# Kernel optimization log

Hardware: AMD Instinct MI355X
Metric: run time of the kernel (lower is better)

The kernel has to match this reference:

```python
import jax, jax.numpy as jnp
import numpy as np
import math

B, Q, C, H, L, P = 8, 900, 256, 8, 4, 4
D = C // H  # head_dim = 32
SPATIAL = np.array([[100, 100], [50, 50], [25, 25], [13, 13]], dtype=np.int64)
AREAS = SPATIAL[:, 0] * SPATIAL[:, 1]
STARTS = np.concatenate([[0], np.cumsum(AREAS)[:-1]]).astype(np.int64)
S = int(AREAS.sum())  # 13294


def _xavier(k, i, o, scale=1.0):
    return jax.random.normal(k, (i, o), jnp.float32) * scale * (2.0 / (i + o)) ** 0.5


def setup_inputs() -> dict:
    key = jax.random.key(0)
    ks = jax.random.split(key, 16)
    inp = {}
    inp['query'] = jax.random.normal(ks[0], (B, Q, C), jnp.float32)
    inp['reference_points'] = jax.random.uniform(ks[1], (B, Q, L, 2), jnp.float32)
    inp['input_flatten'] = jax.random.normal(ks[2], (B, S, C), jnp.float32)
    inp['object_shape'] = jax.random.uniform(ks[3], (B, Q, 2), jnp.float32) * 0.3 + 0.02
    inp['input_spatial_shapes'] = jnp.asarray(SPATIAL)
    inp['input_level_start_index'] = jnp.asarray(STARTS)
    # learned parameters (torch zero-inits offset/attn weights; use small random for a nontrivial baseline)
    inp['w_q'] = _xavier(ks[4], C, C); inp['b_q'] = jnp.zeros((C,), jnp.float32)
    inp['w_v'] = _xavier(ks[5], C, C); inp['b_v'] = jnp.zeros((C,), jnp.float32)
    inp['w_o'] = _xavier(ks[6], C, C); inp['b_o'] = jnp.zeros((C,), jnp.float32)
    inp['w_off1'] = _xavier(ks[7], C + 2, C); inp['b_off1'] = jnp.zeros((C,), jnp.float32)
    inp['w_off2'] = _xavier(ks[8], C, H * L * P * 2, scale=0.05)
    inp['b_off2'] = jax.random.normal(ks[9], (H * L * P * 2,), jnp.float32) * 0.02
    inp['w_ax'] = _xavier(ks[10], C, H * L * P, scale=0.1); inp['b_ax'] = jnp.zeros((H * L * P,), jnp.float32)
    inp['w_ay'] = _xavier(ks[11], C, H * L * P, scale=0.1); inp['b_ay'] = jnp.zeros((H * L * P,), jnp.float32)
    # spectral basis per original init: head h uses freq pi*(h+1)/H over arange(D)
    freq = (np.arange(1, H + 1, dtype=np.float32)[:, None] * math.pi / H) * np.arange(D, dtype=np.float32)[None, :]
    inp['basis_x'] = jnp.asarray(np.cos(freq), jnp.float32)
    inp['basis_y'] = jnp.asarray(np.sin(freq), jnp.float32)
    return inp


def _bilinear_sample(v, locs):
    """v: (B,S,H,D); locs: (B,Q,H,L,P,2) in [0,1]. grid_sample semantics: align_corners=False, zeros padding.
    Returns (B,Q,H,L,P,D)."""
    levels = []
    for lvl in range(L):
        Hl, Wl = int(SPATIAL[lvl, 0]), int(SPATIAL[lvl, 1])
        start = int(STARTS[lvl])
        v_l = v[:, start:start + Hl * Wl]  # (B, Hl*Wl, H, D)
        loc = locs[:, :, :, lvl]  # (B,Q,H,P,2)
        # align_corners=False: pixel coord = loc * size - 0.5
        x = loc[..., 0] * Wl - 0.5
        y = loc[..., 1] * Hl - 0.5
        x0 = jnp.floor(x); y0 = jnp.floor(y)
        fx = x - x0; fy = y - y0
        x0i = x0.astype(jnp.int32); y0i = y0.astype(jnp.int32)
        acc = jnp.zeros((B, Q, H, P, D), jnp.float32)
        corners = [(0, 0, (1 - fx) * (1 - fy)), (1, 0, fx * (1 - fy)),
                   (0, 1, (1 - fx) * fy), (1, 1, fx * fy)]
        for dx, dy, w in corners:
            xi = x0i + dx; yi = y0i + dy
            valid = (xi >= 0) & (xi < Wl) & (yi >= 0) & (yi < Hl)
            idx = jnp.clip(yi, 0, Hl - 1) * Wl + jnp.clip(xi, 0, Wl - 1)  # (B,Q,H,P)
            idx_t = idx.transpose(0, 1, 3, 2).reshape(B, Q * P, H)[..., None]  # (B,Q*P,H,1)
            g = jnp.take_along_axis(v_l, idx_t, axis=1)  # (B,Q*P,H,D)
            g = g.reshape(B, Q, P, H, D).transpose(0, 1, 3, 2, 4)  # (B,Q,H,P,D)
            acc = acc + g * (w * valid.astype(jnp.float32))[..., None]
        levels.append(acc)
    return jnp.stack(levels, axis=3)  # (B,Q,H,L,P,D)


def reference(query, reference_points, input_flatten, input_spatial_shapes, input_level_start_index,
              object_shape, w_q, b_q, w_v, b_v, w_o, b_o, w_off1, b_off1, w_off2, b_off2,
              w_ax, b_ax, w_ay, b_ay, basis_x, basis_y):
    q = query @ w_q + b_q  # (B,Q,C)
    v = (input_flatten @ w_v + b_v).reshape(B, S, H, D)
    q_shape = jnp.concatenate([q, object_shape], axis=-1)  # (B,Q,C+2)
    hid = jax.nn.relu(q_shape @ w_off1 + b_off1)
    offsets = (hid @ w_off2 + b_off2).reshape(B, Q, H, L, P, 2)
    offsets = offsets * object_shape[:, :, None, None, None, :]
    ref = reference_points[:, :, None, :, None, :]  # (B,Q,1,L,1,2)
    locs = jnp.clip(ref + offsets, 0.0, 1.0)  # (B,Q,H,L,P,2)
    q_heads = q.reshape(B, Q, H, D)
    spec = jnp.einsum('bqhd,hd->bqh', q_heads, basis_x) * jnp.einsum('bqhd,hd->bqh', q_heads, basis_y)
    attn_x = (q @ w_ax + b_ax).reshape(B, Q, H, L, P)
    attn_y = (q @ w_ay + b_ay).reshape(B, Q, H, L, P)
    attn = attn_x * attn_y + spec[..., None, None]
    attn = jax.nn.softmax(attn.reshape(B, Q, H, L * P), axis=-1).reshape(B, Q, H, L, P)
    sampled = _bilinear_sample(v, locs)  # (B,Q,H,L,P,D)
    out = (sampled * attn[..., None]).sum(axis=(3, 4)).reshape(B, Q, C)
    return out @ w_o + b_o  # dropout is identity in eval
```

## Files before the change

kernel.cpp:

```cpp
#include <hip/hip_runtime.h>
#include <hip/hip_bf16.h>
#include <math.h>

constexpr int B_ = 8, Q_ = 900;
constexpr int S_ = 13294;
constexpr int BQ = 7200;
constexpr int BS = 106352;

typedef __bf16 bf16x8 __attribute__((ext_vector_type(8)));
typedef float  f32x4  __attribute__((ext_vector_type(4)));

#define WAITLGKM0 asm volatile("s_waitcnt lgkmcnt(0)" ::: "memory")
#define SCHEDB    __builtin_amdgcn_sched_barrier(0)
#define BAR       __builtin_amdgcn_s_barrier()
#define CFENCE    asm volatile("" ::: "memory")

__device__ __forceinline__ void load_lds16(const void* g, void* lds) {
    __builtin_amdgcn_global_load_lds(
        (const __attribute__((address_space(1))) void*)g,
        (__attribute__((address_space(3))) void*)lds, 16, 0, 0);
}

__global__ __launch_bounds__(256)
void transpose_all(const float* __restrict__ wv, const float* __restrict__ wo,
                   const float* __restrict__ woff1, const float* __restrict__ woff2,
                   const float* __restrict__ wax, const float* __restrict__ way,
                   __bf16* __restrict__ tv, __bf16* __restrict__ to_,
                   __bf16* __restrict__ toff2, __bf16* __restrict__ tcat)
{
    const int bi = blockIdx.x;
    __shared__ float tile[32][33];
    const int tx = threadIdx.x & 31, ty = threadIdx.x >> 5;

    const float* src; __bf16* dst; int k0, n0, scol, sN = 256;
    if (bi < 192) {
        const int wid = bi >> 6, t = bi & 63;
        k0 = (t & 7) * 32; n0 = (t >> 3) * 32; scol = n0;
        if      (wid == 0) { src = wv;    dst = tv;    }
        else if (wid == 1) { src = wo;    dst = to_;   }
        else               { src = woff2; dst = toff2; }
    } else {
        const int t = bi - 192;
        k0 = (t & 7) * 32; n0 = (t >> 3) * 32;
        dst = tcat;
        if      (n0 < 128) { src = wax;   scol = n0;       sN = 128; }
        else if (n0 < 256) { src = way;   scol = n0 - 128; sN = 128; }
        else               { src = woff1; scol = n0 - 256; sN = 256; }
    }

    #pragma unroll
    for (int i = 0; i < 4; ++i)
        tile[ty + 8 * i][tx] = src[(size_t)(k0 + ty + 8 * i) * sN + scol + tx];
    __syncthreads();
    #pragma unroll
    for (int i = 0; i < 4; ++i)
        dst[(size_t)(n0 + ty + 8 * i) * 256 + k0 + tx] = (__bf16)tile[tx][ty + 8 * i];
}

__global__ __launch_bounds__(256)
void combine_w(const __bf16* __restrict__ tcat, const float* __restrict__ wq,
               __bf16* __restrict__ wcomb)
{
    const int wid  = (blockIdx.x << 2) + (threadIdx.x >> 6);
    const int lane = threadIdx.x & 63;
    const int n0 = (wid >> 2) * 64, k0 = (wid & 3) * 64;
    const int l15 = lane & 15, l4 = lane >> 4;

    f32x4 acc[4][4] = {};
    #pragma unroll
    for (int s = 0; s < 8; ++s) {
        const int c0 = s * 32 + l4 * 8;
        bf16x8 am[4], bm[4];
        #pragma unroll
        for (int mi = 0; mi < 4; ++mi)
            am[mi] = *(const bf16x8*)(tcat + (size_t)(n0 + mi * 16 + l15) * 256 + c0);
        #pragma unroll
        for (int ni = 0; ni < 4; ++ni) {
            const float* wr_ = wq + (size_t)(k0 + ni * 16 + l15) * 256 + c0;
            const float4 f0 = ((const float4*)wr_)[0];
            const float4 f1 = ((const float4*)wr_)[1];
            bm[ni][0] = (__bf16)f0.x; bm[ni][1] = (__bf16)f0.y;
            bm[ni][2] = (__bf16)f0.z; bm[ni][3] = (__bf16)f0.w;
            bm[ni][4] = (__bf16)f1.x; bm[ni][5] = (__bf16)f1.y;
            bm[ni][6] = (__bf16)f1.z; bm[ni][7] = (__bf16)f1.w;
        }
        #pragma unroll
        for (int mi = 0; mi < 4; ++mi)
            #pragma unroll
            for (int ni = 0; ni < 4; ++ni)
                acc[mi][ni] = __builtin_amdgcn_mfma_f32_16x16x32_bf16(
                    am[mi], bm[ni], acc[mi][ni], 0, 0, 0);
    }
    #pragma unroll
    for (int mi = 0; mi < 4; ++mi)
        #pragma unroll
        for (int rr = 0; rr < 4; ++rr) {
            const int n = n0 + mi * 16 + l4 * 4 + rr;
            #pragma unroll
            for (int ni = 0; ni < 4; ++ni)
                wcomb[(size_t)n * 256 + k0 + ni * 16 + l15] = (__bf16)acc[mi][ni][rr];
        }
}

__global__ __launch_bounds__(256)
void combine_bias(const __bf16* __restrict__ tcat, const float* __restrict__ bq,
                  const float* __restrict__ bax, const float* __restrict__ bay,
                  const float* __restrict__ boff1, float* __restrict__ bcomb)
{
    const int n = blockIdx.x * 256 + threadIdx.x;
    float acc = (n < 128) ? bax[n] : (n < 256 ? bay[n - 128] : boff1[n - 256]);
    const __bf16* row = tcat + (size_t)n * 256;
    #pragma unroll 4
    for (int c8 = 0; c8 < 32; ++c8) {
        const bf16x8 rv = *(const bf16x8*)(row + c8 * 8);
        #pragma unroll
        for (int j = 0; j < 8; ++j) acc += bq[c8 * 8 + j] * (float)rv[j];
    }
    bcomb[n] = acc;
}

__global__ __launch_bounds__(512)
void gemm_v8(const float* __restrict__ A, const __bf16* __restrict__ Wt,
             const float* __restrict__ bias, __bf16* __restrict__ outp, int M)
{
    __shared__ float4 AsbV[2][512];
    __shared__ float4 BsbV[3][1024];
    char* const Asb_b = (char*)AsbV;
    char* const Bsb_b = (char*)BsbV;

    const int tid  = threadIdx.x;
    const int wave = tid >> 6, lane = tid & 63;
    const int wr = wave >> 2, wc = wave & 3;
    const int row0 = blockIdx.x * 128;
    const int l15 = lane & 15, l4 = lane >> 4;

    const int st_row = tid >> 2, st_kq = tid & 3;
    const int gr_cl  = min(row0 + st_row, M - 1);
    const float* Abase = A + (size_t)gr_cl * 256 + st_kq * 8;
    const int a_wo = st_row * 64 + ((st_kq ^ ((st_row >> 1) & 3)) * 16);

    int a_off[4], b_off[4];
    #pragma unroll
    for (int mi = 0; mi < 4; ++mi) {
        const int r = wr * 64 + mi * 16 + l15;
        a_off[mi] = r * 64 + (l4 ^ ((r >> 1) & 3)) * 16;
    }
    #pragma unroll
    for (int ni = 0; ni < 4; ++ni) {
        const int c = wc * 64 + ni * 16 + l15;
        b_off[ni] = c * 64 + (l4 ^ ((c >> 1) & 3)) * 16;
    }

    const __bf16* bsrc[2];
    #pragma unroll
    for (int i = 0; i < 2; ++i) {
        const int c   = (wave * 2 + i) * 64 + lane;
        const int col = c >> 2, kcp = c & 3;
        const int kc  = kcp ^ ((col >> 1) & 3);
        bsrc[i] = Wt + (size_t)col * 256 + kc * 8;
    }

    auto issueB = [&](int kt, int bbuf) {
        #pragma unroll
        for (int i = 0; i < 2; ++i)
            load_lds16(bsrc[i] + kt * 32, Bsb_b + bbuf * 16384 + (wave * 2 + i) * 1024);
    };
    auto loadA = [&](int kt, float4* g) {
        const float* ga = Abase + kt * 32;
        g[0] = ((const float4*)ga)[0];
        g[1] = ((const float4*)ga)[1];
    };
    auto writeA = [&](int abuf, const float4* g) {
        bf16x8 c0;
        c0[0] = (__bf16)g[0].x; c0[1] = (__bf16)g[0].y; c0[2] = (__bf16)g[0].z; c0[3] = (__bf16)g[0].w;
        c0[4] = (__bf16)g[1].x; c0[5] = (__bf16)g[1].y; c0[6] = (__bf16)g[1].z; c0[7] = (__bf16)g[1].w;
        *(bf16x8*)(Asb_b + abuf * 8192 + a_wo) = c0;
    };

    f32x4 acc[4][4] = {};
    float4 g[2][2];

    issueB(0, 0);
    loadA(0, g[0]);
    issueB(1, 1);
    loadA(1, g[1]);
    writeA(0, g[0]);
    WAITLGKM0; BAR; CFENCE; SCHEDB;

    #pragma unroll
    for (int u = 0; u < 8; ++u) {
        if (u + 2 <= 7) {
            loadA(u + 2, g[u & 1]);
            issueB(u + 2, (u + 2) % 3);
        }

        const char* Ab = Asb_b + (u & 1) * 8192;
        const char* Bb = Bsb_b + (u % 3) * 16384;
        bf16x8 a[4], b[4];
        #pragma unroll
        for (int mi = 0; mi < 4; ++mi) a[mi] = *(const bf16x8*)(Ab + a_off[mi]);
        #pragma unroll
        for (int ni = 0; ni < 4; ++ni) b[ni] = *(const bf16x8*)(Bb + b_off[ni]);

        #pragma unroll
        for (int mi = 0; mi < 4; ++mi)
            #pragma unroll
            for (int ni = 0; ni < 4; ++ni)
                acc[mi][ni] = __builtin_amdgcn_mfma_f32_16x16x32_bf16(
                    a[mi], b[ni], acc[mi][ni], 0, 0, 0);

        if (u + 1 <= 7) {
            writeA((u + 1) & 1, g[(u + 1) & 1]);
            WAITLGKM0; BAR; CFENCE; SCHEDB;
        }
    }

    float bb[4];
    #pragma unroll
    for (int ni = 0; ni < 4; ++ni) bb[ni] = bias[wc * 64 + ni * 16 + l15];
    #pragma unroll
    for (int mi = 0; mi < 4; ++mi) {
        #pragma unroll
        for (int rr = 0; rr < 4; ++rr) {
            const int row = row0 + wr * 64 + mi * 16 + l4 * 4 + rr;
            if (row >= M) continue;
            #pragma unroll
            for (int ni = 0; ni < 4; ++ni)
                outp[(size_t)row * 256 + wc * 64 + ni * 16 + l15] =
                    (__bf16)(acc[mi][ni][rr] + bb[ni]);
        }
    }
}

template<bool RELUHI, bool OUTBF16>
__global__ __launch_bounds__(256)
void gemm_dp(const float* __restrict__ A, const __bf16* __restrict__ Wt,
             const float* __restrict__ bias, const float* __restrict__ extra,
             const float* __restrict__ Wex, void* __restrict__ outp,
             int M, int N, int LDA)
{
    __shared__ float4 AsbV[2][512];
    __shared__ float4 BsbV[3][512];
    char* const Asb_b = (char*)AsbV;
    char* const Bsb_b = (char*)BsbV;

    const int tid  = threadIdx.x;
    const int wave = tid >> 6, lane = tid & 63;
    const int wr = wave >> 1, wc = wave & 1;
    const int row0 = blockIdx.y * 128, col0 = blockIdx.x * 128;
    const int l15 = lane & 15, l4 = lane >> 4;

    const int st_row = tid >> 1, st_kh = tid & 1;
    const int gr_cl  = min(row0 + st_row, M - 1);
    const float* Abase = A + (size_t)gr_cl * LDA + st_kh * 16;
    const int asw   = (st_row >> 1) & 3;
    const int a_wo0 = st_row * 64 + ((st_kh * 2)     ^ asw) * 16;
    const int a_wo1 = st_row * 64 + ((st_kh * 2 + 1) ^ asw) * 16;

    int a_off[4], b_off[4];
    #pragma unroll
    for (int mi = 0; mi < 4; ++mi) {
        const int r   = wr * 64 + mi * 16 + l15;
        a_off[mi] = r * 64 + (l4 ^ ((r >> 1) & 3)) * 16;
    }
    #pragma unroll
    for (int ni = 0; ni < 4; ++ni) {
        const int c   = wc * 64 + ni * 16 + l15;
        b_off[ni] = c * 64 + (l4 ^ ((c >> 1) & 3)) * 16;
    }

    const __bf16* bsrc[2];
    #pragma unroll
    for (int i = 0; i < 2; ++i) {
        const int c   = (wave * 2 + i) * 64 + lane;
        const int col = c >> 2, kcp = c & 3;
        const int kc  = kcp ^ ((col >> 1) & 3);
        bsrc[i] = Wt + (size_t)(col0 + col) * 256 + kc * 8;
    }

    auto issueB = [&](int kt, int bbuf) {
        #pragma unroll
        for (int i = 0; i < 2; ++i)
            load_lds16(bsrc[i] + kt * 32, Bsb_b + bbuf * 8192 + (wave * 2 + i) * 1024);
    };
    auto loadA = [&](int kt, float4* g) {
        const float* ga = Abase + kt * 32;
        g[0] = ((const float4*)ga)[0];
        g[1] = ((const float4*)ga)[1];
        g[2] = ((const float4*)ga)[2];
        g[3] = ((const float4*)ga)[3];
    };
    auto writeA = [&](int abuf, const float4* g) {
        bf16x8 c0, c1;
        c0[0] = (__bf16)g[0].x; c0[1] = (__bf16)g[0].y; c0[2] = (__bf16)g[0].z; c0[3] = (__bf16)g[0].w;
        c0[4] = (__bf16)g[1].x; c0[5] = (__bf16)g[1].y; c0[6] = (__bf16)g[1].z; c0[7] = (__bf16)g[1].w;
        c1[0] = (__bf16)g[2].x; c1[1] = (__bf16)g[2].y; c1[2] = (__bf16)g[2].z; c1[3] = (__bf16)g[2].w;
        c1[4] = (__bf16)g[3].x; c1[5] = (__bf16)g[3].y; c1[6] = (__bf16)g[3].z; c1[7] = (__bf16)g[3].w;
        *(bf16x8*)(Asb_b + abuf * 8192 + a_wo0) = c0;
        *(bf16x8*)(Asb_b + abuf * 8192 + a_wo1) = c1;
    };

    f32x4 acc[4][4] = {};
    float4 g[2][4];

    issueB(0, 0);
    loadA(0, g[0]);
    issueB(1, 1);
    loadA(1, g[1]);
    writeA(0, g[0]);
    WAITLGKM0; BAR; CFENCE; SCHEDB;

    #pragma unroll
    for (int u = 0; u < 8; ++u) {
        if (u + 2 <= 7) {
            loadA(u + 2, g[u & 1]);
            issueB(u + 2, (u + 2) % 3);
        }

        const char* Ab = Asb_b + (u & 1) * 8192;
        const char* Bb = Bsb_b + (u % 3) * 8192;
        bf16x8 a[4], b[4];
        #pragma unroll
        for (int mi = 0; mi < 4; ++mi) a[mi] = *(const bf16x8*)(Ab + a_off[mi]);
        #pragma unroll
        for (int ni = 0; ni < 4; ++ni) b[ni] = *(const bf16x8*)(Bb + b_off[ni]);

        #pragma unroll
        for (int mi = 0; mi < 4; ++mi)
            #pragma unroll
            for (int ni = 0; ni < 4; ++ni)
                acc[mi][ni] = __builtin_amdgcn_mfma_f32_16x16x32_bf16(
                    a[mi], b[ni], acc[mi][ni], 0, 0, 0);

        if (u + 1 <= 7) {
            writeA((u + 1) & 1, g[(u + 1) & 1]);
            WAITLGKM0; BAR; CFENCE; SCHEDB;
        }
    }

    int   colb[4];
    float bb[4], we0[4], we1[4];
    #pragma unroll
    for (int ni = 0; ni < 4; ++ni) {
        const int c = col0 + wc * 64 + ni * 16 + l15;
        colb[ni] = c;
        bb[ni]   = bias[c];
        if (RELUHI && c >= 256) { we0[ni] = Wex[c - 256]; we1[ni] = Wex[c - 256 + 256]; }
        else                    { we0[ni] = 0.f; we1[ni] = 0.f; }
    }
    #pragma unroll
    for (int mi = 0; mi < 4; ++mi) {
        #pragma unroll
        for (int rr = 0; rr < 4; ++rr) {
            const int row = row0 + wr * 64 + mi * 16 + l4 * 4 + rr;
            if (row >= M) continue;
            float e0 = 0.f, e1 = 0.f;
            if (RELUHI) { e0 = extra[(size_t)row * 2]; e1 = extra[(size_t)row * 2 + 1]; }
            #pragma unroll
            for (int ni = 0; ni < 4; ++ni) {
                float v = acc[mi][ni][rr] + bb[ni];
                if (RELUHI && colb[ni] >= 256) {
                    v += e0 * we0[ni] + e1 * we1[ni];
                    v = fmaxf(v, 0.f);
                }
                if (OUTBF16) ((__bf16*)outp)[(size_t)row * N + colb[ni]] = (__bf16)v;
                else         ((float*)outp)[(size_t)row * N + colb[ni]]  = v;
            }
        }
    }
}

__global__ __launch_bounds__(256)
void attn_sample_kernel(const float* __restrict__ axyhid,
                        const float* __restrict__ refp, const float* __restrict__ objs,
                        const float* __restrict__ off, const __bf16* __restrict__ v,
                        float* __restrict__ agg)
{
    const int bq = blockIdx.x;
    const int b  = bq / Q_;
    const int tid = threadIdx.x;

    __shared__ float sm[128];
    __shared__ float sa[128];
    __shared__ float sl[256];

    if (tid < 128)
        sm[tid] = axyhid[(size_t)bq * 512 + tid] * axyhid[(size_t)bq * 512 + 128 + tid];
    __syncthreads();

    if (tid < 128) {
        const int hh = tid >> 4;
        float mx = -1e30f;
        #pragma unroll
        for (int i = 0; i < 16; ++i) mx = fmaxf(mx, sm[hh * 16 + i]);
        float s = 0.f;
        #pragma unroll
        for (int i = 0; i < 16; ++i) s += __expf(sm[hh * 16 + i] - mx);
        sa[tid] = __expf(sm[tid] - mx) / s;

        const int l = (tid >> 2) & 3;
        const float os0 = objs[(size_t)bq * 2], os1 = objs[(size_t)bq * 2 + 1];
        const float r0 = refp[((size_t)bq * 4 + l) * 2];
        const float r1 = refp[((size_t)bq * 4 + l) * 2 + 1];
        const float o0 = off[(size_t)bq * 256 + tid * 2]     * os0;
        const float o1 = off[(size_t)bq * 256 + tid * 2 + 1] * os1;
        sl[tid * 2]     = fminf(fmaxf(r0 + o0, 0.f), 1.f);
        sl[tid * 2 + 1] = fminf(fmaxf(r1 + o1, 0.f), 1.f);
    }
    __syncthreads();

    const int h = tid >> 5, lane32 = tid & 31;
    const int sp = lane32 >> 2, cq = lane32 & 3;
    const int chbase = h * 32 + cq * 8;
    const __bf16* vb = v + (size_t)b * S_ * 256;

    float acc8[8] = {};

    #pragma unroll
    for (int gidx = 0; gidx < 2; ++gidx) {
        const int lp  = gidx * 8 + sp;
        const int li  = h * 16 + lp;
        const int lvl = lp >> 2;
        const int Wl = (lvl == 0) ? 100 : (lvl == 1) ? 50 : (lvl == 2) ? 25 : 13;
        const int Hl = Wl;
        const int st = (lvl == 0) ? 0 : (lvl == 1) ? 10000 : (lvl == 2) ? 12500 : 13125;

        const float a  = sa[li];
        const float lx = sl[li * 2], ly = sl[li * 2 + 1];
        const float x = lx * (float)Wl - 0.5f;
        const float y = ly * (float)Hl - 0.5f;
        const float x0f = floorf(x), y0f = floorf(y);
        const float fx = x - x0f, fy = y - y0f;
        const int x0 = (int)x0f, y0 = (int)y0f;

        #pragma unroll
        for (int c = 0; c < 4; ++c) {
            const int dx = c & 1, dy = c >> 1;
            const int xi = x0 + dx, yi = y0 + dy;
            const float wgt = (dx ? fx : 1.f - fx) * (dy ? fy : 1.f - fy);
            const bool valid = (xi >= 0) & (xi < Wl) & (yi >= 0) & (yi < Hl);
            const int idx = min(max(yi, 0), Hl - 1) * Wl + min(max(xi, 0), Wl - 1);
            const float wa = valid ? a * wgt : 0.f;
            const bf16x8 gv = *(const bf16x8*)(vb + (size_t)(st + idx) * 256 + chbase);
            #pragma unroll
            for (int j = 0; j < 8; ++j) acc8[j] += wa * (float)gv[j];
        }
    }

    #pragma unroll
    for (int m = 4; m <= 16; m <<= 1)
        #pragma unroll
        for (int j = 0; j < 8; ++j)
            acc8[j] += __shfl_xor(acc8[j], m);

    if (sp == 0) {
        #pragma unroll
        for (int j = 0; j < 8; ++j)
            agg[(size_t)bq * 256 + chbase + j] = acc8[j];
    }
}

extern "C" void kernel_launch(void* const* d_in, const int* in_sizes, int n_in,
                              void* d_out, int out_size, void* d_ws, size_t ws_size,
                              hipStream_t stream)
{
    const float* query = (const float*)d_in[0];
    const float* refp  = (const float*)d_in[1];
    const float* x_in  = (const float*)d_in[2];
    const float* objs  = (const float*)d_in[3];
    const float* w_q    = (const float*)d_in[6];
    const float* b_q    = (const float*)d_in[7];
    const float* w_v    = (const float*)d_in[8];
    const float* b_v    = (const float*)d_in[9];
    const float* w_o    = (const float*)d_in[10];
    const float* b_o    = (const float*)d_in[11];
    const float* w_off1 = (const float*)d_in[12];
    const float* b_off1 = (const float*)d_in[13];
    const float* w_off2 = (const float*)d_in[14];
    const float* b_off2 = (const float*)d_in[15];
    const float* w_ax   = (const float*)d_in[16];
    const float* b_ax   = (const float*)d_in[17];
    const float* w_ay   = (const float*)d_in[18];
    const float* b_ay   = (const float*)d_in[19];

    float* ws = (float*)d_ws;
    float* axyhid_ws = ws;
    float* off_ws    = axyhid_ws + (size_t)BQ * 512;
    float* agg_ws    = off_ws    + (size_t)BQ * 256;
    float* bcomb_ws  = agg_ws    + (size_t)BQ * 256;
    __bf16* v_bf    = (__bf16*)(bcomb_ws + 512);
    __bf16* wt_v    = v_bf    + (size_t)BS * 256;
    __bf16* wt_o    = wt_v    + 256 * 256;
    __bf16* wt_off2 = wt_o    + 256 * 256;
    __bf16* wt_cat  = wt_off2 + 256 * 256;
    __bf16* wcomb   = wt_cat  + 512 * 256;

    const dim3 blk(256);

    transpose_all<<<320, blk, 0, stream>>>(w_v, w_o, w_off1, w_off2, w_ax, w_ay,
                                           wt_v, wt_o, wt_off2, wt_cat);
    combine_w<<<8, blk, 0, stream>>>(wt_cat, w_q, wcomb);
    combine_bias<<<2, blk, 0, stream>>>(wt_cat, b_q, b_ax, b_ay, b_off1, bcomb_ws);

    gemm_v8<<<(BS + 127) / 128, dim3(512), 0, stream>>>(x_in, wt_v, b_v, v_bf, BS);

    gemm_dp<true, false><<<dim3(4, (BQ + 127) / 128), blk, 0, stream>>>(
        query, wcomb, bcomb_ws, objs, w_off1 + 256 * 256, axyhid_ws, BQ, 512, 256);

    gemm_dp<false, false><<<dim3(2, (BQ + 127) / 128), blk, 0, stream>>>(
        axyhid_ws + 256, wt_off2, b_off2, nullptr, nullptr, off_ws, BQ, 256, 512);

    attn_sample_kernel<<<BQ, blk, 0, stream>>>(axyhid_ws, refp, objs, off_ws,
                                               v_bf, agg_ws);

    gemm_dp<false, false><<<dim3(2, (BQ + 127) / 128), blk, 0, stream>>>(
        agg_ws, wt_o, b_o, nullptr, nullptr, (float*)d_out, BQ, 256, 256);
}
```

Before: 113.2 us.

## Fuse value projection and query GEMM into one launch; merge weight/bias combine kernels

Merges the value-projection GEMM and the combined query/offset-hidden GEMM into a single launch whose blocks pick their work by block index: 831 blocks handle the value projection and 114 blocks handle the query side, split into two column halves. The weight-combine and bias-combine kernels are also merged into one launch. The goal is to cut launch overhead and let the small query GEMM fill the tail of the large value GEMM. In exchange, the query GEMM now runs with the 512-thread, 128x256-tile configuration, and the kernel carries extra branching.

```diff
diff --git a/kernel.cpp b/kernel.cpp
--- a/kernel.cpp
+++ b/kernel.cpp
@@ -6,6 +6,7 @@
 constexpr int S_ = 13294;
 constexpr int BQ = 7200;
 constexpr int BS = 106352;
+constexpr int NVB = 831;
 
 typedef __bf16 bf16x8 __attribute__((ext_vector_type(8)));
 typedef float  f32x4  __attribute__((ext_vector_type(4)));
@@ -58,10 +59,27 @@
 }
 
 __global__ __launch_bounds__(256)
-void combine_w(const __bf16* __restrict__ tcat, const float* __restrict__ wq,
-               __bf16* __restrict__ wcomb)
+void combine2(const __bf16* __restrict__ tcat, const float* __restrict__ wq,
+              const float* __restrict__ bq, const float* __restrict__ bax,
+              const float* __restrict__ bay, const float* __restrict__ boff1,
+              __bf16* __restrict__ wcomb, float* __restrict__ bcomb)
 {
-    const int wid  = (blockIdx.x << 2) + (threadIdx.x >> 6);
+    const int bi = blockIdx.x;
+    if (bi >= 8) {
+        const int n = (bi - 8) * 256 + threadIdx.x;
+        float acc = (n < 128) ? bax[n] : (n < 256 ? bay[n - 128] : boff1[n - 256]);
+        const __bf16* row = tcat + (size_t)n * 256;
+        #pragma unroll 4
+        for (int c8 = 0; c8 < 32; ++c8) {
+            const bf16x8 rv = *(const bf16x8*)(row + c8 * 8);
+            #pragma unroll
+            for (int j = 0; j < 8; ++j) acc += bq[c8 * 8 + j] * (float)rv[j];
+        }
+        bcomb[n] = acc;
+        return;
+    }
+
+    const int wid  = (bi << 2) + (threadIdx.x >> 6);
     const int lane = threadIdx.x & 63;
     const int n0 = (wid >> 2) * 64, k0 = (wid & 3) * 64;
     const int l15 = lane & 15, l4 = lane >> 4;
@@ -102,36 +120,32 @@
         }
 }
 
-__global__ __launch_bounds__(256)
-void combine_bias(const __bf16* __restrict__ tcat, const float* __restrict__ bq,
-                  const float* __restrict__ bax, const float* __restrict__ bay,
-                  const float* __restrict__ boff1, float* __restrict__ bcomb)
-{
-    const int n = blockIdx.x * 256 + threadIdx.x;
-    float acc = (n < 128) ? bax[n] : (n < 256 ? bay[n - 128] : boff1[n - 256]);
-    const __bf16* row = tcat + (size_t)n * 256;
-    #pragma unroll 4
-    for (int c8 = 0; c8 < 32; ++c8) {
-        const bf16x8 rv = *(const bf16x8*)(row + c8 * 8);
-        #pragma unroll
-        for (int j = 0; j < 8; ++j) acc += bq[c8 * 8 + j] * (float)rv[j];
-    }
-    bcomb[n] = acc;
-}
-
 __global__ __launch_bounds__(512)
-void gemm_v8(const float* __restrict__ A, const __bf16* __restrict__ Wt,
-             const float* __restrict__ bias, __bf16* __restrict__ outp, int M)
+void main_fused(const float* __restrict__ x_in, const __bf16* __restrict__ wt_v,
+                const float* __restrict__ b_v, __bf16* __restrict__ v_bf,
+                const float* __restrict__ query, const __bf16* __restrict__ wcomb,
+                const float* __restrict__ bcomb, const float* __restrict__ objs,
+                const float* __restrict__ wex, float* __restrict__ axyhid)
 {
     __shared__ float4 AsbV[2][512];
     __shared__ float4 BsbV[3][1024];
     char* const Asb_b = (char*)AsbV;
     char* const Bsb_b = (char*)BsbV;
 
+    const int bid  = blockIdx.x;
+    const bool isV = (bid < NVB);
+    const int qb   = bid - NVB;
+    const int colhalf = isV ? 0 : (qb & 1);
+
+    const float*  A    = isV ? x_in : query;
+    const __bf16* Wt   = isV ? wt_v : (wcomb + (size_t)colhalf * 256 * 256);
+    const float*  bias = isV ? b_v  : (bcomb + colhalf * 256);
+    const int     M    = isV ? BS   : BQ;
+    const int     row0 = isV ? bid * 128 : (qb >> 1) * 128;
+
     const int tid  = threadIdx.x;
     const int wave = tid >> 6, lane = tid & 63;
     const int wr = wave >> 2, wc = wave & 3;
-    const int row0 = blockIdx.x * 128;
     const int l15 = lane & 15, l4 = lane >> 4;
 
     const int st_row = tid >> 2, st_kq = tid & 3;
@@ -218,25 +232,53 @@
     float bb[4];
     #pragma unroll
     for (int ni = 0; ni < 4; ++ni) bb[ni] = bias[wc * 64 + ni * 16 + l15];
-    #pragma unroll
-    for (int mi = 0; mi < 4; ++mi) {
-        #pragma unroll
-        for (int rr = 0; rr < 4; ++rr) {
-            const int row = row0 + wr * 64 + mi * 16 + l4 * 4 + rr;
-            if (row >= M) continue;
-            #pragma unroll
-            for (int ni = 0; ni < 4; ++ni)
-                outp[(size_t)row * 256 + wc * 64 + ni * 16 + l15] =
-                    (__bf16)(acc[mi][ni][rr] + bb[ni]);
-        }
-    }
-}
-
-template<bool RELUHI, bool OUTBF16>
+
+    if (isV) {
+        #pragma unroll
+        for (int mi = 0; mi < 4; ++mi)
+            #pragma unroll
+            for (int rr = 0; rr < 4; ++rr) {
+                const int row = row0 + wr * 64 + mi * 16 + l4 * 4 + rr;
+                if (row >= M) continue;
+                #pragma unroll
+                for (int ni = 0; ni < 4; ++ni)
+                    v_bf[(size_t)row * 256 + wc * 64 + ni * 16 + l15] =
+                        (__bf16)(acc[mi][ni][rr] + bb[ni]);
+            }
+    } else {
+        float we0[4], we1[4];
+        #pragma unroll
+        for (int ni = 0; ni < 4; ++ni) {
+            const int c = wc * 64 + ni * 16 + l15;
+            we0[ni] = colhalf ? wex[c]       : 0.f;
+            we1[ni] = colhalf ? wex[256 + c] : 0.f;
+        }
+        #pragma unroll
+        for (int mi = 0; mi < 4; ++mi)
+            #pragma unroll
+            for (int rr = 0; rr < 4; ++rr) {
+                const int row = row0 + wr * 64 + mi * 16 + l4 * 4 + rr;
+                if (row >= M) continue;
+                const float e0 = objs[(size_t)row * 2];
+                const float e1 = objs[(size_t)row * 2 + 1];
+                #pragma unroll
+                for (int ni = 0; ni < 4; ++ni) {
+                    const int c = wc * 64 + ni * 16 + l15;
+                    float v = acc[mi][ni][rr] + bb[ni];
+                    if (colhalf) {
+                        v += e0 * we0[ni] + e1 * we1[ni];
+                        v = fmaxf(v, 0.f);
+                    }
+                    axyhid[(size_t)row * 512 + colhalf * 256 + c] = v;
+                }
+            }
+    }
+}
+
+template<bool OUTBF16>
 __global__ __launch_bounds__(256)
 void gemm_dp(const float* __restrict__ A, const __bf16* __restrict__ Wt,
-             const float* __restrict__ bias, const float* __restrict__ extra,
-             const float* __restrict__ Wex, void* __restrict__ outp,
+             const float* __restrict__ bias, void* __restrict__ outp,
              int M, int N, int LDA)
 {
     __shared__ float4 AsbV[2][512];
@@ -338,33 +380,21 @@
         }
     }
 
-    int   colb[4];
-    float bb[4], we0[4], we1[4];
-    #pragma unroll
-    for (int ni = 0; ni < 4; ++ni) {
-        const int c = col0 + wc * 64 + ni * 16 + l15;
-        colb[ni] = c;
-        bb[ni]   = bias[c];
-        if (RELUHI && c >= 256) { we0[ni] = Wex[c - 256]; we1[ni] = Wex[c - 256 + 256]; }
-        else                    { we0[ni] = 0.f; we1[ni] = 0.f; }
-    }
+    float bb[4];
+    #pragma unroll
+    for (int ni = 0; ni < 4; ++ni) bb[ni] = bias[col0 + wc * 64 + ni * 16 + l15];
     #pragma unroll
     for (int mi = 0; mi < 4; ++mi) {
         #pragma unroll
         for (int rr = 0; rr < 4; ++rr) {
             const int row = row0 + wr * 64 + mi * 16 + l4 * 4 + rr;
             if (row >= M) continue;
-            float e0 = 0.f, e1 = 0.f;
-            if (RELUHI) { e0 = extra[(size_t)row * 2]; e1 = extra[(size_t)row * 2 + 1]; }
             #pragma unroll
             for (int ni = 0; ni < 4; ++ni) {
-                float v = acc[mi][ni][rr] + bb[ni];
-                if (RELUHI && colb[ni] >= 256) {
-                    v += e0 * we0[ni] + e1 * we1[ni];
-                    v = fmaxf(v, 0.f);
-                }
-                if (OUTBF16) ((__bf16*)outp)[(size_t)row * N + colb[ni]] = (__bf16)v;
-                else         ((float*)outp)[(size_t)row * N + colb[ni]]  = v;
+                const float v = acc[mi][ni][rr] + bb[ni];
+                const int colb = col0 + wc * 64 + ni * 16 + l15;
+                if (OUTBF16) ((__bf16*)outp)[(size_t)row * N + colb] = (__bf16)v;
+                else         ((float*)outp)[(size_t)row * N + colb]  = v;
             }
         }
     }
@@ -499,20 +529,19 @@
 
     transpose_all<<<320, blk, 0, stream>>>(w_v, w_o, w_off1, w_off2, w_ax, w_ay,
                                            wt_v, wt_o, wt_off2, wt_cat);
-    combine_w<<<8, blk, 0, stream>>>(wt_cat, w_q, wcomb);
-    combine_bias<<<2, blk, 0, stream>>>(wt_cat, b_q, b_ax, b_ay, b_off1, bcomb_ws);
-
-    gemm_v8<<<(BS + 127) / 128, dim3(512), 0, stream>>>(x_in, wt_v, b_v, v_bf, BS);
-
-    gemm_dp<true, false><<<dim3(4, (BQ + 127) / 128), blk, 0, stream>>>(
-        query, wcomb, bcomb_ws, objs, w_off1 + 256 * 256, axyhid_ws, BQ, 512, 256);
-
-    gemm_dp<false, false><<<dim3(2, (BQ + 127) / 128), blk, 0, stream>>>(
-        axyhid_ws + 256, wt_off2, b_off2, nullptr, nullptr, off_ws, BQ, 256, 512);
+    combine2<<<10, blk, 0, stream>>>(wt_cat, w_q, b_q, b_ax, b_ay, b_off1,
+                                     wcomb, bcomb_ws);
+
+    main_fused<<<NVB + 114, dim3(512), 0, stream>>>(
+        x_in, wt_v, b_v, v_bf,
+        query, wcomb, bcomb_ws, objs, w_off1 + 256 * 256, axyhid_ws);
+
+    gemm_dp<false><<<dim3(2, (BQ + 127) / 128), blk, 0, stream>>>(
+        axyhid_ws + 256, wt_off2, b_off2, off_ws, BQ, 256, 512);
 
     attn_sample_kernel<<<BQ, blk, 0, stream>>>(axyhid_ws, refp, objs, off_ws,
                                                v_bf, agg_ws);
 
-    gemm_dp<false, false><<<dim3(2, (BQ + 127) / 128), blk, 0, stream>>>(
-        agg_ws, wt_o, b_o, nullptr, nullptr, (float*)d_out, BQ, 256, 256);
-}
+    gemm_dp<false><<<dim3(2, (BQ + 127) / 128), blk, 0, stream>>>(
+        agg_ws, wt_o, b_o, (float*)d_out, BQ, 256, 256);
+}
```

New measurement: 106.6 us. 1.06x faster.
